# Kernel optimization log

Measured on AMD Instinct MI355X. Metric: run time of the kernel, lower is better.

Reference implementation:

```python
import jax, jax.numpy as jnp
import numpy as np

B = 128      # graphs
N = 32       # atoms per graph (fixed)
NODES = B * N
E = B * N * N  # fully-connected edges incl. self-loops
H = 256      # hidden_dim
TD = 128     # time_dim
TYPE = 100   # type_dim
NF = 10      # frac_emb_freq
EDGE_DIM = NF * 2 * 3 + 6  # 66
L = 4        # num_layers
EPS = 1e-5


def _edges():
    idx = jnp.arange(NODES).reshape(B, N)
    ei = jnp.broadcast_to(idx[:, :, None], (B, N, N)).reshape(-1)  # row (target)
    ej = jnp.broadcast_to(idx[:, None, :], (B, N, N)).reshape(-1)  # col (source)
    return ei, ej


def _layernorm(x, g, b):
    mu = jnp.mean(x, axis=-1, keepdims=True)
    var = jnp.mean((x - mu) ** 2, axis=-1, keepdims=True)
    return (x - mu) * jax.lax.rsqrt(var + EPS) * g + b


def setup_inputs() -> dict:
    key = jax.random.key(0)
    ks = jax.random.split(key, 32)
    p = lambda k, shp: (jax.random.normal(k, shp, dtype=jnp.float32) * 0.02)
    inp = {
        "t": jax.random.uniform(ks[0], (B,), dtype=jnp.float32),
        "atom_types": jax.random.normal(ks[1], (NODES, TYPE), dtype=jnp.float32),
        "frac_coords": jax.random.uniform(ks[2], (NODES, 3), dtype=jnp.float32),
        "l_polar": jax.random.normal(ks[3], (B, 6), dtype=jnp.float32),
        "node2graph": jnp.repeat(jnp.arange(B, dtype=jnp.int32), N),
        # type_smooth
        "Ws": p(ks[4], (TYPE, H)), "bs": jnp.zeros((H,), jnp.float32),
        # node_embedding
        "Wn": p(ks[5], (H + TD, H)), "bn": jnp.zeros((H,), jnp.float32),
        # per-layer params, stacked over L
        "ln_g": jnp.ones((L, H), jnp.float32), "ln_b": jnp.zeros((L, H), jnp.float32),
        "m1_W": p(ks[6], (L, 2 * H + EDGE_DIM, H)), "m1_b": jnp.zeros((L, H), jnp.float32),
        "m2_W": p(ks[7], (L, H, H)), "m2_b": jnp.zeros((L, H), jnp.float32),
        "a1_W": p(ks[8], (L, 2 * H, H)), "a1_b": jnp.zeros((L, H), jnp.float32),
        "a2_W": p(ks[9], (L, H, H)), "a2_b": jnp.zeros((L, H), jnp.float32),
        # final layer norm + readouts
        "fln_g": jnp.ones((H,), jnp.float32), "fln_b": jnp.zeros((H,), jnp.float32),
        "type_W": p(ks[10], (H, TYPE)), "type_b": jnp.zeros((TYPE,), jnp.float32),
        "polar_W": p(ks[11], (H, 6)),
        "frac_W": p(ks[12], (H, 3)),
    }
    return inp


def reference(t, atom_types, frac_coords, l_polar, node2graph,
              Ws, bs, Wn, bn, ln_g, ln_b, m1_W, m1_b, m2_W, m2_b,
              a1_W, a1_b, a2_W, a2_b, fln_g, fln_b, type_W, type_b,
              polar_W, frac_W):
    ei, ej = _edges()
    edge2graph = node2graph[ei]

    # ---- node features: type_smooth + sinusoidal time embedding ----
    half = TD // 2
    tfreq = jnp.exp(jnp.arange(half, dtype=jnp.float32) * (-np.log(10000.0) / (half - 1)))
    targ = t[:, None] * tfreq[None, :]                       # [B, half]
    time_emb = jnp.concatenate([jnp.sin(targ), jnp.cos(targ)], axis=-1)  # [B, TD]
    time_emb = jnp.repeat(time_emb, N, axis=0)               # [NODES, TD]
    type_emb = atom_types @ Ws + bs                           # [NODES, H]
    nf = jnp.concatenate([type_emb, time_emb], axis=-1) @ Wn + bn  # [NODES, H]

    # ---- edge features: sinusoidal frac-diff embedding + l_polar ----
    d = jnp.mod(frac_coords[ej] - frac_coords[ei], 1.0)       # [E, 3]
    ffreq = 2.0 * np.pi * jnp.arange(NF, dtype=jnp.float32)
    femb = (d[:, :, None] * ffreq[None, None, :]).reshape(E, NF * 3)
    femb = jnp.concatenate([jnp.sin(femb), jnp.cos(femb)], axis=-1)  # [E, 60]
    ef = jnp.concatenate([femb, l_polar[edge2graph]], axis=-1)       # [E, 66]

    # ---- GNN layers ----
    ones = jnp.ones((E,), jnp.float32)
    cnt = jax.ops.segment_sum(ones, ei, num_segments=NODES)          # [NODES]
    cnt = jnp.maximum(cnt, 1.0)[:, None]
    for i in range(L):
        h = _layernorm(nf, ln_g[i], ln_b[i])
        mij = jnp.concatenate([h[ei], h[ej], ef], axis=-1)           # [E, 2H+66]
        mij = jax.nn.silu(mij @ m1_W[i] + m1_b[i])
        mij = jax.nn.silu(mij @ m2_W[i] + m2_b[i])                   # [E, H]
        msg = jax.ops.segment_sum(mij, ei, num_segments=NODES) / cnt  # scatter-mean
        a = jnp.concatenate([nf, msg], axis=-1)
        a = jax.nn.silu(a @ a1_W[i] + a1_b[i])
        a = jax.nn.silu(a @ a2_W[i] + a2_b[i])
        nf = nf + a

    nf = _layernorm(nf, fln_g, fln_b)
    gsum = jax.ops.segment_sum(nf, node2graph, num_segments=B)
    gcnt = jnp.maximum(jax.ops.segment_sum(jnp.ones((NODES,), jnp.float32), node2graph, num_segments=B), 1.0)
    graph_features = gsum / gcnt[:, None]

    type_pred = nf @ type_W + type_b
    l_polar_pred = graph_features @ polar_W
    frac_coords_pred = nf @ frac_W
    return type_pred, l_polar_pred, frac_coords_pred
```

## Files before the change

### kernel.cpp

```cpp
#include <hip/hip_runtime.h>
#include <hip/hip_bf16.h>

typedef __attribute__((ext_vector_type(8))) short short8;
typedef __attribute__((ext_vector_type(4))) short short4v;
typedef __attribute__((ext_vector_type(4))) float float4v;
typedef __bf16 bf16x8 __attribute__((ext_vector_type(8)));

#define MFMA16(A,B,C) __builtin_amdgcn_mfma_f32_16x16x32_bf16( \
    __builtin_bit_cast(bf16x8,(A)), __builtin_bit_cast(bf16x8,(B)), (C), 0, 0, 0)

static __device__ __forceinline__ float bf2f(unsigned short b){
  unsigned u = ((unsigned)b) << 16; float f; __builtin_memcpy(&f,&u,sizeof(f)); return f;
}
static __device__ __forceinline__ unsigned short f2bf(float f){
  __bf16 h = (__bf16)f;
  return __builtin_bit_cast(unsigned short, h);
}
static __device__ __forceinline__ float siluf(float x){
  return x * __builtin_amdgcn_rcpf(1.0f + __expf(-x));
}
static __device__ __forceinline__ float ldf(const float* p, size_t i){ return p[i]; }
static __device__ __forceinline__ float ldf(const unsigned short* p, size_t i){ return bf2f(p[i]); }

static __device__ __forceinline__ void gemm_body(
    const unsigned short* __restrict__ A, int lda,
    const unsigned short* __restrict__ Bp, int KT, int NT,
    const float* __restrict__ bias,
    float* __restrict__ outF, int ldoF,
    unsigned short* __restrict__ outH, int ldoH,
    const float* __restrict__ res,
    int Nc, int flags, int bx, int by)
{
  const int w = threadIdx.x >> 6, lane = threadIdx.x & 63;
  const int l15 = lane & 15, q = lane >> 4;
  const int rowL = bx * 64 + w * 16;
  const int colB = by * 64;
  const short8* pa = (const short8*)(A + (size_t)(rowL + l15) * lda);
  const short8* pb = (const short8*)Bp;
  float4v acc[4] = {};
  int ntc[4];
  #pragma unroll
  for (int i = 0; i < 4; ++i){ int t = (colB >> 4) + i; ntc[i] = t < NT ? t : NT - 1; }
  for (int kt = 0; kt < KT; ++kt){
    short8 a = pa[kt * 4 + q];
    #pragma unroll
    for (int i = 0; i < 4; ++i){
      short8 b = pb[(size_t)(kt * NT + ntc[i]) * 64 + lane];
      acc[i] = MFMA16(a, b, acc[i]);
    }
  }
  const bool doB = flags & 2, doS = flags & 1, doR = flags & 4;
  #pragma unroll
  for (int i = 0; i < 4; ++i){
    int c = colB + i * 16 + l15;
    if (c >= Nc) continue;
    float bv = doB ? bias[c] : 0.0f;
    #pragma unroll
    for (int r = 0; r < 4; ++r){
      int row = rowL + q * 4 + r;
      float v = acc[i][r] + bv;
      if (doS) v = siluf(v);
      if (doR) v += res[(size_t)row * ldoF + c];
      if (outF) outF[(size_t)row * ldoF + c] = v;
      if (outH) outH[(size_t)row * ldoH + c] = f2bf(v);
    }
  }
}

__global__ __launch_bounds__(256) void k_gemm(
    const unsigned short* __restrict__ A, int lda,
    const unsigned short* __restrict__ Bp, int KT, int NT,
    const float* __restrict__ bias,
    float* __restrict__ outF, int ldoF,
    unsigned short* __restrict__ outH, int ldoH,
    const float* __restrict__ res,
    int Nc, int flags)
{
  gemm_body(A, lda, Bp, KT, NT, bias, outF, ldoF, outH, ldoH, res, Nc, flags,
            blockIdx.x, blockIdx.y);
}

template<typename T>
static __device__ __forceinline__ void pack_tile(
    const T* W, int ldw, int Krows, int Ncols,
    unsigned short* dst, int NTtot, int ntoff, int kt, int nt,
    const float* addrow, int lane)
{
  int l15 = lane & 15, q = lane >> 4;
  int col = nt * 16 + l15;
  int kr0 = kt * 32 + q * 8;
  short8 v;
  #pragma unroll
  for (int j = 0; j < 8; ++j){
    int r = kr0 + j;
    float x = 0.0f;
    if (r < Krows && col < Ncols){
      x = ldf(W, (size_t)r * ldw + col);
      if (addrow) x += addrow[(r >> 5) * 256 + col];
    }
    v[j] = (short)f2bf(x);
  }
  ((short8*)dst)[(size_t)(kt * NTtot + ntoff + nt) * 64 + lane] = v;
}

static __device__ __forceinline__ void packW_dispatch(
    int b, int lane,
    const float* Ws, const float* Wn,
    const float* typeW, const float* polarW, const float* fracW,
    const float* m1W, const float* m2W, const float* a1W, const float* a2W,
    unsigned short* Wsp, unsigned short* Wnp, unsigned short* typep,
    unsigned short* polarp, unsigned short* fracp,
    unsigned short* W12p, unsigned short* W1botp, unsigned short* W2Tp,
    unsigned short* a1p, unsigned short* a2p)
{
  if (b < 64)      { pack_tile(Ws,    256, 100, 256, Wsp,   16, 0, b >> 4, b & 15, nullptr, lane); return; }
  if (b < 256){ int s = b - 64;  pack_tile(Wn,    256, 384, 256, Wnp,   16, 0, s >> 4, s & 15, nullptr, lane); return; }
  if (b < 312){ int s = b - 256; pack_tile(typeW, 100, 256, 100, typep,  7, 0, s / 7,  s % 7,  nullptr, lane); return; }
  if (b < 320){ int s = b - 312; pack_tile(polarW,  6, 256,   6, polarp, 1, 0, s, 0, nullptr, lane); return; }
  if (b < 328){ int s = b - 320; pack_tile(fracW,   3, 256,   3, fracp,  1, 0, s, 0, nullptr, lane); return; }
  int s2 = b - 328;
  int l = s2 / 800, bb = s2 % 800;
  const float* m1Wl = m1W + (size_t)l * 578 * 256;
  const float* m2Wl = m2W + (size_t)l * 65536;
  const float* a1Wl = a1W + (size_t)l * 131072;
  const float* a2Wl = a2W + (size_t)l * 65536;
  unsigned short* W12pl   = W12p   + (size_t)l * 131072;
  unsigned short* W1botpl = W1botp + (size_t)l * 16384;
  unsigned short* W2Tpl   = W2Tp   + (size_t)l * 65536;
  unsigned short* a1pl    = a1p    + (size_t)l * 131072;
  unsigned short* a2pl    = a2p    + (size_t)l * 65536;
  if (bb < 128)       pack_tile(m1Wl,           256, 256, 256, W12pl,  32,  0, bb >> 4, bb & 15, nullptr, lane);
  else if (bb < 256){ int s = bb - 128; pack_tile(m1Wl + 256*256, 256, 256, 256, W12pl,  32, 16, s >> 4, s & 15, nullptr, lane); }
  else if (bb < 288){ int s = bb - 256; pack_tile(m1Wl + 512*256, 256,  64, 256, W1botpl,16,  0, s >> 4, s & 15, nullptr, lane); }
  else if (bb < 416){ int s = bb - 288; pack_tile(m2Wl,           256, 256, 256, W2Tpl,  16,  0, s >> 4, s & 15, nullptr, lane); }
  else if (bb < 672){ int s = bb - 416; pack_tile(a1Wl,           256, 512, 256, a1pl,   16,  0, s >> 4, s & 15, nullptr, lane); }
  else              { int s = bb - 672; pack_tile(a2Wl,           256, 256, 256, a2pl,   16,  0, s >> 4, s & 15, nullptr, lane); }
}

__global__ void k_prep(
    const float* Ws, const float* Wn,
    const float* typeW, const float* polarW, const float* fracW,
    const float* m1W, const float* m2W, const float* a1W, const float* a2W,
    unsigned short* Wsp, unsigned short* Wnp, unsigned short* typep,
    unsigned short* polarp, unsigned short* fracp,
    unsigned short* W12p, unsigned short* W1botp, unsigned short* W2Tp,
    unsigned short* a1p, unsigned short* a2p,
    const float* at, const float* t, const float* fc,
    const float* lpol, const float* m1b,
    unsigned short* atp, unsigned short* cat1,
    unsigned short* femb, float* lpw)
{
  int b0 = blockIdx.x;
  if (b0 < 882){
    int tile = b0 * 4 + (threadIdx.x >> 6);
    packW_dispatch(tile, threadIdx.x & 63, Ws, Wn, typeW, polarW, fracW,
                   m1W, m2W, a1W, a2W, Wsp, Wnp, typep, polarp, fracp,
                   W12p, W1botp, W2Tp, a1p, a2p);
    return;
  }
  int b = b0 - 882;
  if (b < 2048){
    int id = b * 256 + threadIdx.x;
    int r = id >> 7, c = id & 127;
    atp[id] = (c < 100) ? f2bf(at[r * 100 + c]) : (unsigned short)0;
  } else if (b < 2176){
    int g = b - 2048, i = threadIdx.x;
    if (i < 128){
      float tg = t[g];
      int f = i & 63;
      float fr = __expf((-9.210340371976184f / 63.0f) * (float)f);
      float arg = tg * fr;
      float v = (i < 64) ? __sinf(arg) : __cosf(arg);
      unsigned short hv = f2bf(v);
      for (int n = 0; n < 32; ++n)
        cat1[(size_t)(g * 32 + n) * 384 + 256 + i] = hv;
    }
  } else if (b < 2688){
    int e = (b - 2176) * 256 + threadIdx.x;
    int g = e >> 10, i = (e >> 5) & 31, j = e & 31;
    int nt = g * 32 + i, ns = g * 32 + j;
    unsigned short o[64];
    #pragma unroll
    for (int k = 0; k < 3; ++k){
      float d = fc[ns * 3 + k] - fc[nt * 3 + k];
      d -= floorf(d);
      #pragma unroll
      for (int f = 0; f < 10; ++f){
        float ang = d * (6.283185307179586f * (float)f);
        o[k * 10 + f]      = f2bf(__sinf(ang));
        o[30 + k * 10 + f] = f2bf(__cosf(ang));
      }
    }
    #pragma unroll
    for (int z = 60; z < 64; ++z) o[z] = 0;
    short8* dst = (short8*)femb;
    int eb = e >> 4, l15e = e & 15;
    #pragma unroll
    for (int ks = 0; ks < 2; ++ks)
      #pragma unroll
      for (int qq = 0; qq < 4; ++qq){
        short8 s;
        #pragma unroll
        for (int j2 = 0; j2 < 8; ++j2) s[j2] = (short)o[(ks*4+qq)*8 + j2];
        dst[((size_t)(eb*2 + ks))*64 + qq*16 + l15e] = s;
      }
  } else {
    int s = b - 2688;
    int l = s >> 7, g = s & 127, c = threadIdx.x;
    const float* W = m1W + (size_t)l * 578 * 256;
    float acc = m1b[l * 256 + c];
    #pragma unroll
    for (int k = 0; k < 6; ++k)
      acc += lpol[g * 6 + k] * W[(572 + k) * 256 + c];
    lpw[((size_t)l * 128 + g) * 256 + c] = acc;
  }
}

#define HLD 264

__global__ __launch_bounds__(256) void k_lnP(
    const float* __restrict__ nf, const float* __restrict__ g_,
    const float* __restrict__ b_,
    const unsigned short* __restrict__ W12p, const float* __restrict__ lpwl,
    unsigned short* __restrict__ P1, unsigned short* __restrict__ P2)
{
  __shared__ unsigned short hld[32 * HLD];
  const int w = threadIdx.x >> 6, lane = threadIdx.x & 63;
  const int l15 = lane & 15, q = lane >> 4;
  const int g = blockIdx.x >> 2, q4 = blockIdx.x & 3;
  #pragma unroll
  for (int rr = 0; rr < 8; ++rr){
    int row = w * 8 + rr;
    float4v x = *(const float4v*)(nf + ((size_t)(g*32+row))*256 + lane*4);
    float s = x[0]+x[1]+x[2]+x[3];
    #pragma unroll
    for (int m=1;m<64;m<<=1) s += __shfl_xor(s,m,64);
    float mu = s * (1.f/256.f);
    float d0=x[0]-mu,d1=x[1]-mu,d2=x[2]-mu,d3=x[3]-mu;
    float vs=d0*d0+d1*d1+d2*d2+d3*d3;
    #pragma unroll
    for (int m=1;m<64;m<<=1) vs += __shfl_xor(vs,m,64);
    float rs = rsqrtf(vs*(1.f/256.f)+1e-5f);
    float4v gg = *(const float4v*)(g_ + lane*4);
    float4v bb = *(const float4v*)(b_ + lane*4);
    short4v o;
    o[0]=(short)f2bf(d0*rs*gg[0]+bb[0]);
    o[1]=(short)f2bf(d1*rs*gg[1]+bb[1]);
    o[2]=(short)f2bf(d2*rs*gg[2]+bb[2]);
    o[3]=(short)f2bf(d3*rs*gg[3]+bb[3]);
    *(short4v*)(&hld[row*HLD + lane*4]) = o;
  }
  __syncthreads();
  float4v acc[2][2] = {};
  const short8* pb = (const short8*)W12p;
  for (int kt = 0; kt < 8; ++kt){
    short8 a0 = *(const short8*)(&hld[(size_t)l15*HLD + kt*32 + q*8]);
    short8 a1 = *(const short8*)(&hld[(size_t)(16+l15)*HLD + kt*32 + q*8]);
    #pragma unroll
    for (int i = 0; i < 2; ++i){
      short8 bfr = pb[(size_t)(kt*32 + q4*8 + w*2 + i)*64 + lane];
      acc[0][i] = MFMA16(a0, bfr, acc[0][i]);
      acc[1][i] = MFMA16(a1, bfr, acc[1][i]);
    }
  }
  unsigned short* dst = (q4 < 2) ? P1 : P2;
  const int cho = (q4 & 1) * 128;
  #pragma unroll
  for (int i = 0; i < 2; ++i){
    int ch = cho + (w*2 + i)*16 + l15;
    float lv = (q4 < 2) ? lpwl[g*256 + ch] : 0.0f;
    #pragma unroll
    for (int mt = 0; mt < 2; ++mt){
      #pragma unroll
      for (int r = 0; r < 4; ++r){
        int node = g*32 + mt*16 + q*4 + r;
        dst[(size_t)node*256 + ch] = f2bf(acc[mt][i][r] + lv);
      }
    }
  }
}

__global__ __launch_bounds__(512) void k_a12P(
    const unsigned short* __restrict__ cat2,
    const unsigned short* __restrict__ a1pl, const float* __restrict__ a1bl,
    const unsigned short* __restrict__ a2pl, const float* __restrict__ a2bl,
    float* __restrict__ nf, unsigned short* __restrict__ cat2w,
    const float* __restrict__ lng, const float* __restrict__ lnb,
    const unsigned short* __restrict__ W12p, const float* __restrict__ lpwl,
    unsigned short* __restrict__ P1, unsigned short* __restrict__ P2, int doP)
{
  __shared__ float nf32[16 * 260];
  __shared__ unsigned short sh[16 * HLD];
  const int w = threadIdx.x >> 6, lane = threadIdx.x & 63;
  const int l15 = lane & 15, q = lane >> 4;
  const int r0 = blockIdx.x * 16;
  const int g = blockIdx.x >> 1;
  const short8* pb1 = (const short8*)a1pl;
  const short8* pb2 = (const short8*)a2pl;
  float4v acc[2] = {};
  for (int kt = 0; kt < 16; ++kt){
    short8 a0 = *(const short8*)(cat2 + (size_t)(r0 + l15)*512 + kt*32 + q*8);
    #pragma unroll
    for (int i = 0; i < 2; ++i){
      short8 bfr = pb1[(size_t)(kt*16 + w*2 + i)*64 + lane];
      acc[i] = MFMA16(a0, bfr, acc[i]);
    }
  }
  #pragma unroll
  for (int i = 0; i < 2; ++i){
    int c = (w*2+i)*16 + l15;
    float bv = a1bl[c];
    #pragma unroll
    for (int r = 0; r < 4; ++r)
      sh[(size_t)(q*4 + r)*HLD + c] = f2bf(siluf(acc[i][r] + bv));
  }
  __syncthreads();
  float4v c2[2] = {};
  for (int kt = 0; kt < 8; ++kt){
    short8 a0 = *(const short8*)(&sh[(size_t)l15*HLD + kt*32 + q*8]);
    #pragma unroll
    for (int i = 0; i < 2; ++i){
      short8 bfr = pb2[(size_t)(kt*16 + w*2 + i)*64 + lane];
      c2[i] = MFMA16(a0, bfr, c2[i]);
    }
  }
  #pragma unroll
  for (int i = 0; i < 2; ++i){
    int c = (w*2+i)*16 + l15;
    float bv = a2bl[c];
    #pragma unroll
    for (int r = 0; r < 4; ++r){
      int row = r0 + q*4 + r;
      float v = nf[(size_t)row*256 + c] + siluf(c2[i][r] + bv);
      nf[(size_t)row*256 + c] = v;
      cat2w[(size_t)row*512 + c] = f2bf(v);
      nf32[(q*4 + r)*260 + c] = v;
    }
  }
  if (!doP) return;
  __syncthreads();
  #pragma unroll
  for (int rr = 0; rr < 2; ++rr){
    int row = w * 2 + rr;
    float4v x = *(const float4v*)(&nf32[row*260 + lane*4]);
    float s = x[0]+x[1]+x[2]+x[3];
    #pragma unroll
    for (int m=1;m<64;m<<=1) s += __shfl_xor(s,m,64);
    float mu = s * (1.f/256.f);
    float d0=x[0]-mu,d1=x[1]-mu,d2=x[2]-mu,d3=x[3]-mu;
    float vs=d0*d0+d1*d1+d2*d2+d3*d3;
    #pragma unroll
    for (int m=1;m<64;m<<=1) vs += __shfl_xor(vs,m,64);
    float rs = rsqrtf(vs*(1.f/256.f)+1e-5f);
    float4v gg = *(const float4v*)(lng + lane*4);
    float4v bb = *(const float4v*)(lnb + lane*4);
    short4v o;
    o[0]=(short)f2bf(d0*rs*gg[0]+bb[0]);
    o[1]=(short)f2bf(d1*rs*gg[1]+bb[1]);
    o[2]=(short)f2bf(d2*rs*gg[2]+bb[2]);
    o[3]=(short)f2bf(d3*rs*gg[3]+bb[3]);
    *(short4v*)(&sh[row*HLD + lane*4]) = o;
  }
  __syncthreads();
  float4v pc[4] = {};
  const short8* pb = (const short8*)W12p;
  for (int kt = 0; kt < 8; ++kt){
    short8 a0 = *(const short8*)(&sh[(size_t)l15*HLD + kt*32 + q*8]);
    #pragma unroll
    for (int i = 0; i < 4; ++i){
      short8 bfr = pb[(size_t)(kt*32 + w*4 + i)*64 + lane];
      pc[i] = MFMA16(a0, bfr, pc[i]);
    }
  }
  #pragma unroll
  for (int i = 0; i < 4; ++i){
    int nt = w*4 + i;
    unsigned short* dst = (nt < 16) ? P1 : P2;
    int ch = (nt & 15)*16 + l15;
    float lv = (nt < 16) ? lpwl[g*256 + ch] : 0.0f;
    #pragma unroll
    for (int r = 0; r < 4; ++r){
      int node = r0 + q*4 + r;
      dst[(size_t)node*256 + ch] = f2bf(pc[i][r] + lv);
    }
  }
}

__global__ __launch_bounds__(256) void k_lnFO(
    const float* __restrict__ nf, const float* __restrict__ g_,
    const float* __restrict__ b_,
    const unsigned short* __restrict__ typep, const float* __restrict__ typeb,
    const unsigned short* __restrict__ polarp,
    const unsigned short* __restrict__ fracp,
    float* __restrict__ out)
{
  __shared__ unsigned short hld[33 * HLD];
  const int w = threadIdx.x >> 6, lane = threadIdx.x & 63;
  const int l15 = lane & 15, q = lane >> 4;
  const int g = blockIdx.x >> 1, h = blockIdx.x & 1;
  #pragma unroll
  for (int rr = 0; rr < 8; ++rr){
    int row = w * 8 + rr;
    float4v x = *(const float4v*)(nf + ((size_t)(g*32+row))*256 + lane*4);
    float s = x[0]+x[1]+x[2]+x[3];
    #pragma unroll
    for (int m=1;m<64;m<<=1) s += __shfl_xor(s,m,64);
    float mu = s * (1.f/256.f);
    float d0=x[0]-mu,d1=x[1]-mu,d2=x[2]-mu,d3=x[3]-mu;
    float vs=d0*d0+d1*d1+d2*d2+d3*d3;
    #pragma unroll
    for (int m=1;m<64;m<<=1) vs += __shfl_xor(vs,m,64);
    float rs = rsqrtf(vs*(1.f/256.f)+1e-5f);
    float4v gg = *(const float4v*)(g_ + lane*4);
    float4v bb = *(const float4v*)(b_ + lane*4);
    short4v o;
    o[0]=(short)f2bf(d0*rs*gg[0]+bb[0]);
    o[1]=(short)f2bf(d1*rs*gg[1]+bb[1]);
    o[2]=(short)f2bf(d2*rs*gg[2]+bb[2]);
    o[3]=(short)f2bf(d3*rs*gg[3]+bb[3]);
    *(short4v*)(&hld[row*HLD + lane*4]) = o;
  }
  __syncthreads();
  {
    int c = threadIdx.x;
    float s = 0.0f;
    #pragma unroll
    for (int n = 0; n < 32; ++n) s += bf2f(hld[n*HLD + c]);
    hld[32*HLD + c] = f2bf(s * (1.0f/32.0f));
  }
  __syncthreads();
  {
    float4v tacc[2] = {};
    const short8* pb = (const short8*)typep;
    for (int kt = 0; kt < 8; ++kt){
      short8 a0 = *(const short8*)(&hld[(size_t)(h*16 + l15)*HLD + kt*32 + q*8]);
      #pragma unroll
      for (int i = 0; i < 2; ++i){
        int nt = w + i*4; if (nt > 6) nt = 6;
        short8 bfr = pb[(size_t)(kt*7 + nt)*64 + lane];
        tacc[i] = MFMA16(a0, bfr, tacc[i]);
      }
    }
    #pragma unroll
    for (int i = 0; i < 2; ++i){
      int c = (w + i*4)*16 + l15;
      if (c < 100){
        float bv = typeb[c];
        #pragma unroll
        for (int r = 0; r < 4; ++r){
          int node = g*32 + h*16 + q*4 + r;
          out[(size_t)node*100 + c] = tacc[i][r] + bv;
        }
      }
    }
  }
  if (w == 0){
    float4v facc = {};
    const short8* pb = (const short8*)fracp;
    for (int kt = 0; kt < 8; ++kt){
      short8 a0 = *(const short8*)(&hld[(size_t)(h*16 + l15)*HLD + kt*32 + q*8]);
      facc = MFMA16(a0, pb[(size_t)kt*64 + lane], facc);
    }
    if (l15 < 3){
      #pragma unroll
      for (int r = 0; r < 4; ++r){
        int node = g*32 + h*16 + q*4 + r;
        out[410368 + (size_t)node*3 + l15] = facc[r];
      }
    }
  }
  if (h == 1 && w == 3){
    float4v pacc = {};
    const short8* pb = (const short8*)polarp;
    for (int kt = 0; kt < 8; ++kt){
      short8 a0 = *(const short8*)(&hld[(size_t)32*HLD + kt*32 + q*8]);
      pacc = MFMA16(a0, pb[(size_t)kt*64 + lane], pacc);
    }
    if (q == 0 && l15 < 6)
      out[409600 + (size_t)g*6 + l15] = pacc[0];
  }
}

#define EST 268
__global__ __launch_bounds__(256, 4) void k_edge(
    const unsigned short* __restrict__ femb,
    const unsigned short* __restrict__ W1botp,
    const unsigned short* __restrict__ P1,
    const unsigned short* __restrict__ P2,
    const unsigned short* __restrict__ W2Tp,
    const float* __restrict__ b2,
    unsigned short* __restrict__ cat2)
{
  __shared__ unsigned short M1[64 * EST];
  const int w = threadIdx.x >> 6, lane = threadIdx.x & 63;
  const int l15 = lane & 15, q = lane >> 4;
  const int b = blockIdx.x, g = b >> 4;
  const int n0 = (b & 15) * 2;
  const int cb = w * 64;
  const short8* fb8  = (const short8*)femb;
  const short8* w1b8 = (const short8*)W1botp;
  const short8* w2t8 = (const short8*)W2Tp;

  short4v p1v[2][4], p2v[2][4];
  #pragma unroll
  for (int ct = 0; ct < 4; ++ct){
    int co = cb + ct*16 + q*4;
    p1v[0][ct] = *(const short4v*)(P1 + (size_t)(g*32 + n0    )*256 + co);
    p1v[1][ct] = *(const short4v*)(P1 + (size_t)(g*32 + n0 + 1)*256 + co);
    p2v[0][ct] = *(const short4v*)(P2 + (size_t)(g*32 +      l15)*256 + co);
    p2v[1][ct] = *(const short4v*)(P2 + (size_t)(g*32 + 16 + l15)*256 + co);
  }

  float4v acc[4][4] = {};
  #pragma unroll
  for (int ks = 0; ks < 2; ++ks){
    short8 a[4];
    #pragma unroll
    for (int ct = 0; ct < 4; ++ct)
      a[ct] = w1b8[(size_t)(ks * 16 + w * 4 + ct) * 64 + lane];
    #pragma unroll
    for (int et = 0; et < 4; ++et){
      short8 bf = fb8[((size_t)((b*4 + et)*2 + ks))*64 + lane];
      #pragma unroll
      for (int ct = 0; ct < 4; ++ct)
        acc[ct][et] = MFMA16(a[ct], bf, acc[ct][et]);
    }
  }
  #pragma unroll
  for (int ct = 0; ct < 4; ++ct)
    #pragma unroll
    for (int et = 0; et < 4; ++et){
      short4v sv;
      #pragma unroll
      for (int r = 0; r < 4; ++r){
        float v = acc[ct][et][r] + bf2f(p1v[et>>1][ct][r]) + bf2f(p2v[et&1][ct][r]);
        sv[r] = (short)f2bf(siluf(v));
      }
      *(short4v*)(&M1[(size_t)(et * 16 + l15) * EST + cb + ct * 16 + q * 4]) = sv;
    }
  __syncthreads();
  float4v c2[4][4] = {};
  for (int kt = 0; kt < 8; ++kt){
    short8 a[4];
    #pragma unroll
    for (int ct = 0; ct < 4; ++ct)
      a[ct] = w2t8[(size_t)(kt * 16 + w * 4 + ct) * 64 + lane];
    #pragma unroll
    for (int et = 0; et < 4; ++et){
      short8 m = *(const short8*)(&M1[(size_t)(et * 16 + l15) * EST + kt * 32 + q * 8]);
      #pragma unroll
      for (int ct = 0; ct < 4; ++ct)
        c2[ct][et] = MFMA16(m, a[ct], c2[ct][et]);
    }
  }
  #pragma unroll
  for (int ct = 0; ct < 4; ++ct){
    float bv = b2[cb + ct * 16 + l15];
    #pragma unroll
    for (int nn = 0; nn < 2; ++nn){
      float s = siluf(c2[ct][2*nn  ][0] + bv) + siluf(c2[ct][2*nn  ][1] + bv)
              + siluf(c2[ct][2*nn  ][2] + bv) + siluf(c2[ct][2*nn  ][3] + bv)
              + siluf(c2[ct][2*nn+1][0] + bv) + siluf(c2[ct][2*nn+1][1] + bv)
              + siluf(c2[ct][2*nn+1][2] + bv) + siluf(c2[ct][2*nn+1][3] + bv);
      s += __shfl_xor(s, 16, 64);
      s += __shfl_xor(s, 32, 64);
      if (q == 0)
        cat2[(size_t)(b*2 + nn) * 512 + 256 + cb + ct * 16 + l15] =
            f2bf(s * (1.0f / 32.0f));
    }
  }
}

extern "C" void kernel_launch(void* const* d_in, const int* in_sizes, int n_in,
                              void* d_out, int out_size, void* d_ws, size_t ws_size,
                              hipStream_t stream)
{
  const float* t      = (const float*)d_in[0];
  const float* at     = (const float*)d_in[1];
  const float* fc     = (const float*)d_in[2];
  const float* lpol   = (const float*)d_in[3];
  const float* Ws     = (const float*)d_in[5];
  const float* bs     = (const float*)d_in[6];
  const float* Wn     = (const float*)d_in[7];
  const float* bn     = (const float*)d_in[8];
  const float* ln_g   = (const float*)d_in[9];
  const float* ln_b   = (const float*)d_in[10];
  const float* m1W    = (const float*)d_in[11];
  const float* m1b    = (const float*)d_in[12];
  const float* m2W    = (const float*)d_in[13];
  const float* m2b    = (const float*)d_in[14];
  const float* a1W    = (const float*)d_in[15];
  const float* a1b    = (const float*)d_in[16];
  const float* a2W    = (const float*)d_in[17];
  const float* a2b    = (const float*)d_in[18];
  const float* flng   = (const float*)d_in[19];
  const float* flnb   = (const float*)d_in[20];
  const float* typeW  = (const float*)d_in[21];
  const float* typeb  = (const float*)d_in[22];
  const float* polarW = (const float*)d_in[23];
  const float* fracW  = (const float*)d_in[24];
  float* out = (float*)d_out;

  char* ws = (char*)d_ws;
  size_t off = 0;
  auto alloc = [&](size_t bytes) -> char* {
    char* p = ws + off; off += (bytes + 255) & ~(size_t)255; return p;
  };
  float*          nf    = (float*)         alloc((size_t)4096*256*4);
  unsigned short* cat2  = (unsigned short*)alloc((size_t)4096*512*2);
  unsigned short* cat1  = (unsigned short*)alloc((size_t)4096*384*2);
  unsigned short* atp   = (unsigned short*)alloc((size_t)4096*128*2);
  unsigned short* femb  = (unsigned short*)alloc((size_t)131072*64*2);
  float*          lpw   = (float*)         alloc((size_t)4*128*256*4);
  unsigned short* P1    = (unsigned short*)alloc((size_t)4096*256*2);
  unsigned short* P2    = (unsigned short*)alloc((size_t)4096*256*2);
  unsigned short* Wsp   = (unsigned short*)alloc((size_t)4*16*1024);
  unsigned short* Wnp   = (unsigned short*)alloc((size_t)12*16*1024);
  unsigned short* typep = (unsigned short*)alloc((size_t)8*7*1024);
  unsigned short* polarp= (unsigned short*)alloc((size_t)8*1*1024);
  unsigned short* fracp = (unsigned short*)alloc((size_t)8*1*1024);
  unsigned short* W12p  = (unsigned short*)alloc((size_t)4*131072*2);
  unsigned short* W1botp= (unsigned short*)alloc((size_t)4*16384*2);
  unsigned short* W2Tp  = (unsigned short*)alloc((size_t)4*65536*2);
  unsigned short* a1p   = (unsigned short*)alloc((size_t)4*131072*2);
  unsigned short* a2p   = (unsigned short*)alloc((size_t)4*65536*2);

  k_prep<<<dim3(4082), dim3(256), 0, stream>>>(Ws, Wn, typeW, polarW, fracW,
      m1W, m2W, a1W, a2W,
      Wsp, Wnp, typep, polarp, fracp, W12p, W1botp, W2Tp, a1p, a2p,
      at, t, fc, lpol, m1b, atp, cat1, femb, lpw);
  k_gemm<<<dim3(64,4), dim3(256), 0, stream>>>(atp, 128, Wsp, 4, 16, bs,
      (float*)nullptr, 0, cat1, 384, (const float*)nullptr, 256, 2);
  k_gemm<<<dim3(64,4), dim3(256), 0, stream>>>(cat1, 384, Wnp, 12, 16, bn,
      nf, 256, cat2, 512, (const float*)nullptr, 256, 2);
  k_lnP<<<dim3(512), dim3(256), 0, stream>>>(nf, ln_g, ln_b, W12p, lpw, P1, P2);

  for (int l = 0; l < 4; ++l){
    int ln = (l + 1 < 4) ? l + 1 : 3;
    k_edge<<<dim3(2048), dim3(256), 0, stream>>>(femb, W1botp + (size_t)l*16384,
        P1, P2, W2Tp + (size_t)l*65536, m2b + l*256, cat2);
    k_a12P<<<dim3(256), dim3(512), 0, stream>>>(cat2, a1p + (size_t)l*131072,
        a1b + l*256, a2p + (size_t)l*65536, a2b + l*256, nf, cat2,
        ln_g + ln*256, ln_b + ln*256, W12p + (size_t)ln*131072,
        lpw + (size_t)ln*32768, P1, P2, (l < 3) ? 1 : 0);
  }

  k_lnFO<<<dim3(256), dim3(256), 0, stream>>>(nf, flng, flnb,
      typep, typeb, polarp, fracp, out);
}
```

Baseline: 335.0 us.

## Fuse atom-type embedding, node embedding and first LayerNorm projection into one kernel

Replaces the two k_gemm launches and k_lnP with one k_embed kernel. Each block handles 16 nodes and keeps the bf16 atom-type and cat1 tiles in shared memory, computing the time embedding in-block. It then runs both embedding GEMMs, the LayerNorm and the P1/P2 projection without global round-trips. k_prep shrinks because it no longer converts atom types or writes cat1. This saves launches and intermediate global traffic, but k_embed has only 256 blocks and each re-reads the full packed weight matrices.

```diff
diff --git a/kernel.cpp b/kernel.cpp
--- a/kernel.cpp
+++ b/kernel.cpp
@@ -21,64 +21,6 @@
 }
 static __device__ __forceinline__ float ldf(const float* p, size_t i){ return p[i]; }
 static __device__ __forceinline__ float ldf(const unsigned short* p, size_t i){ return bf2f(p[i]); }
-
-static __device__ __forceinline__ void gemm_body(
-    const unsigned short* __restrict__ A, int lda,
-    const unsigned short* __restrict__ Bp, int KT, int NT,
-    const float* __restrict__ bias,
-    float* __restrict__ outF, int ldoF,
-    unsigned short* __restrict__ outH, int ldoH,
-    const float* __restrict__ res,
-    int Nc, int flags, int bx, int by)
-{
-  const int w = threadIdx.x >> 6, lane = threadIdx.x & 63;
-  const int l15 = lane & 15, q = lane >> 4;
-  const int rowL = bx * 64 + w * 16;
-  const int colB = by * 64;
-  const short8* pa = (const short8*)(A + (size_t)(rowL + l15) * lda);
-  const short8* pb = (const short8*)Bp;
-  float4v acc[4] = {};
-  int ntc[4];
-  #pragma unroll
-  for (int i = 0; i < 4; ++i){ int t = (colB >> 4) + i; ntc[i] = t < NT ? t : NT - 1; }
-  for (int kt = 0; kt < KT; ++kt){
-    short8 a = pa[kt * 4 + q];
-    #pragma unroll
-    for (int i = 0; i < 4; ++i){
-      short8 b = pb[(size_t)(kt * NT + ntc[i]) * 64 + lane];
-      acc[i] = MFMA16(a, b, acc[i]);
-    }
-  }
-  const bool doB = flags & 2, doS = flags & 1, doR = flags & 4;
-  #pragma unroll
-  for (int i = 0; i < 4; ++i){
-    int c = colB + i * 16 + l15;
-    if (c >= Nc) continue;
-    float bv = doB ? bias[c] : 0.0f;
-    #pragma unroll
-    for (int r = 0; r < 4; ++r){
-      int row = rowL + q * 4 + r;
-      float v = acc[i][r] + bv;
-      if (doS) v = siluf(v);
-      if (doR) v += res[(size_t)row * ldoF + c];
-      if (outF) outF[(size_t)row * ldoF + c] = v;
-      if (outH) outH[(size_t)row * ldoH + c] = f2bf(v);
-    }
-  }
-}
-
-__global__ __launch_bounds__(256) void k_gemm(
-    const unsigned short* __restrict__ A, int lda,
-    const unsigned short* __restrict__ Bp, int KT, int NT,
-    const float* __restrict__ bias,
-    float* __restrict__ outF, int ldoF,
-    unsigned short* __restrict__ outH, int ldoH,
-    const float* __restrict__ res,
-    int Nc, int flags)
-{
-  gemm_body(A, lda, Bp, KT, NT, bias, outF, ldoF, outH, ldoH, res, Nc, flags,
-            blockIdx.x, blockIdx.y);
-}
 
 template<typename T>
 static __device__ __forceinline__ void pack_tile(
@@ -145,9 +87,7 @@
     unsigned short* polarp, unsigned short* fracp,
     unsigned short* W12p, unsigned short* W1botp, unsigned short* W2Tp,
     unsigned short* a1p, unsigned short* a2p,
-    const float* at, const float* t, const float* fc,
-    const float* lpol, const float* m1b,
-    unsigned short* atp, unsigned short* cat1,
+    const float* fc, const float* lpol, const float* m1b,
     unsigned short* femb, float* lpw)
 {
   int b0 = blockIdx.x;
@@ -159,79 +99,136 @@
     return;
   }
   int b = b0 - 882;
-  if (b < 2048){
-    int id = b * 256 + threadIdx.x;
-    int r = id >> 7, c = id & 127;
-    atp[id] = (c < 100) ? f2bf(at[r * 100 + c]) : (unsigned short)0;
-  } else if (b < 2176){
-    int g = b - 2048, i = threadIdx.x;
-    if (i < 128){
+  if (b < 512){
+    int e = b * 256 + threadIdx.x;
+    int g = e >> 10, i = (e >> 5) & 31, j = e & 31;
+    int nt = g * 32 + i, ns = g * 32 + j;
+    unsigned short o[64];
+    #pragma unroll
+    for (int k = 0; k < 3; ++k){
+      float d = fc[ns * 3 + k] - fc[nt * 3 + k];
+      d -= floorf(d);
+      #pragma unroll
+      for (int f = 0; f < 10; ++f){
+        float ang = d * (6.283185307179586f * (float)f);
+        o[k * 10 + f]      = f2bf(__sinf(ang));
+        o[30 + k * 10 + f] = f2bf(__cosf(ang));
+      }
+    }
+    #pragma unroll
+    for (int z = 60; z < 64; ++z) o[z] = 0;
+    short8* dst = (short8*)femb;
+    int eb = e >> 4, l15e = e & 15;
+    #pragma unroll
+    for (int ks = 0; ks < 2; ++ks)
+      #pragma unroll
+      for (int qq = 0; qq < 4; ++qq){
+        short8 s;
+        #pragma unroll
+        for (int j2 = 0; j2 < 8; ++j2) s[j2] = (short)o[(ks*4+qq)*8 + j2];
+        dst[((size_t)(eb*2 + ks))*64 + qq*16 + l15e] = s;
+      }
+  } else {
+    int s = b - 512;
+    int l = s >> 7, g = s & 127, c = threadIdx.x;
+    const float* W = m1W + (size_t)l * 578 * 256;
+    float acc = m1b[l * 256 + c];
+    #pragma unroll
+    for (int k = 0; k < 6; ++k)
+      acc += lpol[g * 6 + k] * W[(572 + k) * 256 + c];
+    lpw[((size_t)l * 128 + g) * 256 + c] = acc;
+  }
+}
+
+#define HLD 264
+
+__global__ __launch_bounds__(256) void k_embed(
+    const float* __restrict__ at, const float* __restrict__ t,
+    const unsigned short* __restrict__ Wsp, const float* __restrict__ bs,
+    const unsigned short* __restrict__ Wnp, const float* __restrict__ bn,
+    const float* __restrict__ lng, const float* __restrict__ lnb,
+    const unsigned short* __restrict__ W12p, const float* __restrict__ lpwl,
+    float* __restrict__ nf, unsigned short* __restrict__ cat2w,
+    unsigned short* __restrict__ P1, unsigned short* __restrict__ P2)
+{
+  __shared__ unsigned short at_s[16 * 136];
+  __shared__ unsigned short cat1_s[16 * 392];
+  __shared__ float nf32[16 * 260];
+  __shared__ unsigned short sh[16 * HLD];
+  const int w = threadIdx.x >> 6, lane = threadIdx.x & 63;
+  const int l15 = lane & 15, q = lane >> 4;
+  const int r0 = blockIdx.x * 16, g = blockIdx.x >> 1;
+  {
+    int row = threadIdx.x & 15, c0 = (threadIdx.x >> 4) * 8;
+    #pragma unroll
+    for (int j = 0; j < 8; ++j){
+      int c = c0 + j;
+      at_s[row*136 + c] = (c < 100) ? f2bf(at[(size_t)(r0+row)*100 + c])
+                                    : (unsigned short)0;
+    }
+    if (threadIdx.x < 128){
+      int i = threadIdx.x;
       float tg = t[g];
       int f = i & 63;
       float fr = __expf((-9.210340371976184f / 63.0f) * (float)f);
       float arg = tg * fr;
       float v = (i < 64) ? __sinf(arg) : __cosf(arg);
       unsigned short hv = f2bf(v);
-      for (int n = 0; n < 32; ++n)
-        cat1[(size_t)(g * 32 + n) * 384 + 256 + i] = hv;
-    }
-  } else if (b < 2688){
-    int e = (b - 2176) * 256 + threadIdx.x;
-    int g = e >> 10, i = (e >> 5) & 31, j = e & 31;
-    int nt = g * 32 + i, ns = g * 32 + j;
-    unsigned short o[64];
-    #pragma unroll
-    for (int k = 0; k < 3; ++k){
-      float d = fc[ns * 3 + k] - fc[nt * 3 + k];
-      d -= floorf(d);
-      #pragma unroll
-      for (int f = 0; f < 10; ++f){
-        float ang = d * (6.283185307179586f * (float)f);
-        o[k * 10 + f]      = f2bf(__sinf(ang));
-        o[30 + k * 10 + f] = f2bf(__cosf(ang));
-      }
-    }
-    #pragma unroll
-    for (int z = 60; z < 64; ++z) o[z] = 0;
-    short8* dst = (short8*)femb;
-    int eb = e >> 4, l15e = e & 15;
-    #pragma unroll
-    for (int ks = 0; ks < 2; ++ks)
-      #pragma unroll
-      for (int qq = 0; qq < 4; ++qq){
-        short8 s;
-        #pragma unroll
-        for (int j2 = 0; j2 < 8; ++j2) s[j2] = (short)o[(ks*4+qq)*8 + j2];
-        dst[((size_t)(eb*2 + ks))*64 + qq*16 + l15e] = s;
-      }
-  } else {
-    int s = b - 2688;
-    int l = s >> 7, g = s & 127, c = threadIdx.x;
-    const float* W = m1W + (size_t)l * 578 * 256;
-    float acc = m1b[l * 256 + c];
-    #pragma unroll
-    for (int k = 0; k < 6; ++k)
-      acc += lpol[g * 6 + k] * W[(572 + k) * 256 + c];
-    lpw[((size_t)l * 128 + g) * 256 + c] = acc;
-  }
-}
-
-#define HLD 264
-
-__global__ __launch_bounds__(256) void k_lnP(
-    const float* __restrict__ nf, const float* __restrict__ g_,
-    const float* __restrict__ b_,
-    const unsigned short* __restrict__ W12p, const float* __restrict__ lpwl,
-    unsigned short* __restrict__ P1, unsigned short* __restrict__ P2)
-{
-  __shared__ unsigned short hld[32 * HLD];
-  const int w = threadIdx.x >> 6, lane = threadIdx.x & 63;
-  const int l15 = lane & 15, q = lane >> 4;
-  const int g = blockIdx.x >> 2, q4 = blockIdx.x & 3;
-  #pragma unroll
-  for (int rr = 0; rr < 8; ++rr){
-    int row = w * 8 + rr;
-    float4v x = *(const float4v*)(nf + ((size_t)(g*32+row))*256 + lane*4);
+      for (int n = 0; n < 16; ++n) cat1_s[n*392 + 256 + i] = hv;
+    }
+  }
+  __syncthreads();
+  {
+    float4v acc[4] = {};
+    const short8* pb = (const short8*)Wsp;
+    for (int kt = 0; kt < 4; ++kt){
+      short8 a0 = *(const short8*)(&at_s[l15*136 + kt*32 + q*8]);
+      #pragma unroll
+      for (int i = 0; i < 4; ++i){
+        short8 bfr = pb[(size_t)(kt*16 + w*4 + i)*64 + lane];
+        acc[i] = MFMA16(a0, bfr, acc[i]);
+      }
+    }
+    #pragma unroll
+    for (int i = 0; i < 4; ++i){
+      int c = (w*4+i)*16 + l15;
+      float bv = bs[c];
+      #pragma unroll
+      for (int r = 0; r < 4; ++r)
+        cat1_s[(q*4+r)*392 + c] = f2bf(acc[i][r] + bv);
+    }
+  }
+  __syncthreads();
+  {
+    float4v acc[4] = {};
+    const short8* pb = (const short8*)Wnp;
+    for (int kt = 0; kt < 12; ++kt){
+      short8 a0 = *(const short8*)(&cat1_s[l15*392 + kt*32 + q*8]);
+      #pragma unroll
+      for (int i = 0; i < 4; ++i){
+        short8 bfr = pb[(size_t)(kt*16 + w*4 + i)*64 + lane];
+        acc[i] = MFMA16(a0, bfr, acc[i]);
+      }
+    }
+    #pragma unroll
+    for (int i = 0; i < 4; ++i){
+      int c = (w*4+i)*16 + l15;
+      float bv = bn[c];
+      #pragma unroll
+      for (int r = 0; r < 4; ++r){
+        int row = r0 + q*4 + r;
+        float v = acc[i][r] + bv;
+        nf[(size_t)row*256 + c] = v;
+        cat2w[(size_t)row*512 + c] = f2bf(v);
+        nf32[(q*4+r)*260 + c] = v;
+      }
+    }
+  }
+  __syncthreads();
+  #pragma unroll
+  for (int rr = 0; rr < 4; ++rr){
+    int row = w * 4 + rr;
+    float4v x = *(const float4v*)(&nf32[row*260 + lane*4]);
     float s = x[0]+x[1]+x[2]+x[3];
     #pragma unroll
     for (int m=1;m<64;m<<=1) s += __shfl_xor(s,m,64);
@@ -241,41 +238,36 @@
     #pragma unroll
     for (int m=1;m<64;m<<=1) vs += __shfl_xor(vs,m,64);
     float rs = rsqrtf(vs*(1.f/256.f)+1e-5f);
-    float4v gg = *(const float4v*)(g_ + lane*4);
-    float4v bb = *(const float4v*)(b_ + lane*4);
+    float4v gg = *(const float4v*)(lng + lane*4);
+    float4v bb = *(const float4v*)(lnb + lane*4);
     short4v o;
     o[0]=(short)f2bf(d0*rs*gg[0]+bb[0]);
     o[1]=(short)f2bf(d1*rs*gg[1]+bb[1]);
     o[2]=(short)f2bf(d2*rs*gg[2]+bb[2]);
     o[3]=(short)f2bf(d3*rs*gg[3]+bb[3]);
-    *(short4v*)(&hld[row*HLD + lane*4]) = o;
-  }
-  __syncthreads();
-  float4v acc[2][2] = {};
+    *(short4v*)(&sh[row*HLD + lane*4]) = o;
+  }
+  __syncthreads();
+  float4v pc[8] = {};
   const short8* pb = (const short8*)W12p;
   for (int kt = 0; kt < 8; ++kt){
-    short8 a0 = *(const short8*)(&hld[(size_t)l15*HLD + kt*32 + q*8]);
-    short8 a1 = *(const short8*)(&hld[(size_t)(16+l15)*HLD + kt*32 + q*8]);
-    #pragma unroll
-    for (int i = 0; i < 2; ++i){
-      short8 bfr = pb[(size_t)(kt*32 + q4*8 + w*2 + i)*64 + lane];
-      acc[0][i] = MFMA16(a0, bfr, acc[0][i]);
-      acc[1][i] = MFMA16(a1, bfr, acc[1][i]);
-    }
-  }
-  unsigned short* dst = (q4 < 2) ? P1 : P2;
-  const int cho = (q4 & 1) * 128;
-  #pragma unroll
-  for (int i = 0; i < 2; ++i){
-    int ch = cho + (w*2 + i)*16 + l15;
-    float lv = (q4 < 2) ? lpwl[g*256 + ch] : 0.0f;
-    #pragma unroll
-    for (int mt = 0; mt < 2; ++mt){
-      #pragma unroll
-      for (int r = 0; r < 4; ++r){
-        int node = g*32 + mt*16 + q*4 + r;
-        dst[(size_t)node*256 + ch] = f2bf(acc[mt][i][r] + lv);
-      }
+    short8 a0 = *(const short8*)(&sh[(size_t)l15*HLD + kt*32 + q*8]);
+    #pragma unroll
+    for (int i = 0; i < 8; ++i){
+      short8 bfr = pb[(size_t)(kt*32 + w*8 + i)*64 + lane];
+      pc[i] = MFMA16(a0, bfr, pc[i]);
+    }
+  }
+  #pragma unroll
+  for (int i = 0; i < 8; ++i){
+    int nt = w*8 + i;
+    unsigned short* dst = (nt < 16) ? P1 : P2;
+    int ch = (nt & 15)*16 + l15;
+    float lv = (nt < 16) ? lpwl[g*256 + ch] : 0.0f;
+    #pragma unroll
+    for (int r = 0; r < 4; ++r){
+      int node = r0 + q*4 + r;
+      dst[(size_t)node*256 + ch] = f2bf(pc[i][r] + lv);
     }
   }
 }
@@ -608,8 +600,6 @@
   };
   float*          nf    = (float*)         alloc((size_t)4096*256*4);
   unsigned short* cat2  = (unsigned short*)alloc((size_t)4096*512*2);
-  unsigned short* cat1  = (unsigned short*)alloc((size_t)4096*384*2);
-  unsigned short* atp   = (unsigned short*)alloc((size_t)4096*128*2);
   unsigned short* femb  = (unsigned short*)alloc((size_t)131072*64*2);
   float*          lpw   = (float*)         alloc((size_t)4*128*256*4);
   unsigned short* P1    = (unsigned short*)alloc((size_t)4096*256*2);
@@ -625,15 +615,12 @@
   unsigned short* a1p   = (unsigned short*)alloc((size_t)4*131072*2);
   unsigned short* a2p   = (unsigned short*)alloc((size_t)4*65536*2);
 
-  k_prep<<<dim3(4082), dim3(256), 0, stream>>>(Ws, Wn, typeW, polarW, fracW,
+  k_prep<<<dim3(1906), dim3(256), 0, stream>>>(Ws, Wn, typeW, polarW, fracW,
       m1W, m2W, a1W, a2W,
       Wsp, Wnp, typep, polarp, fracp, W12p, W1botp, W2Tp, a1p, a2p,
-      at, t, fc, lpol, m1b, atp, cat1, femb, lpw);
-  k_gemm<<<dim3(64,4), dim3(256), 0, stream>>>(atp, 128, Wsp, 4, 16, bs,
-      (float*)nullptr, 0, cat1, 384, (const float*)nullptr, 256, 2);
-  k_gemm<<<dim3(64,4), dim3(256), 0, stream>>>(cat1, 384, Wnp, 12, 16, bn,
-      nf, 256, cat2, 512, (const float*)nullptr, 256, 2);
-  k_lnP<<<dim3(512), dim3(256), 0, stream>>>(nf, ln_g, ln_b, W12p, lpw, P1, P2);
+      fc, lpol, m1b, femb, lpw);
+  k_embed<<<dim3(256), dim3(256), 0, stream>>>(at, t, Wsp, bs, Wnp, bn,
+      ln_g, ln_b, W12p, lpw, nf, cat2, P1, P2);
 
   for (int l = 0; l < 4; ++l){
     int ln = (l + 1 < 4) ? l + 1 : 3;
```

After: 333.7 us. No clear change (-0.4%).
